# Kernel optimization log

Hardware: AMD Instinct MI355X
Metric: run time of the kernel (lower is better)

## Reference

```python
import jax, jax.numpy as jnp
import numpy as np

D_MODEL = 512
NHEAD = 8
HEAD_DIM = D_MODEL // NHEAD
D_FF = 2048
EPS = 1e-5


def _linear_params(key, d_in, d_out):
    kw, kb = jax.random.split(key)
    bound = 1.0 / np.sqrt(d_in)
    W = jax.random.uniform(kw, (d_out, d_in), jnp.float32, -bound, bound)
    b = jax.random.uniform(kb, (d_out,), jnp.float32, -bound, bound)
    return W, b


def setup_inputs() -> dict:
    key = jax.random.key(0)
    ks = jax.random.split(key, 8)
    src = jax.random.normal(ks[0], (4, 2048, D_MODEL), jnp.float32)
    Wq, bq = _linear_params(ks[1], D_MODEL, D_MODEL)
    Wk, bk = _linear_params(ks[2], D_MODEL, D_MODEL)
    Wv, bv = _linear_params(ks[3], D_MODEL, D_MODEL)
    Wo, bo = _linear_params(ks[4], D_MODEL, D_MODEL)
    W1, b1 = _linear_params(ks[5], D_MODEL, D_FF)
    W2, b2 = _linear_params(ks[6], D_FF, D_MODEL)
    g1 = jnp.ones((D_MODEL,), jnp.float32)
    be1 = jnp.zeros((D_MODEL,), jnp.float32)
    g2 = jnp.ones((D_MODEL,), jnp.float32)
    be2 = jnp.zeros((D_MODEL,), jnp.float32)
    return dict(src=src, Wq=Wq, bq=bq, Wk=Wk, bk=bk, Wv=Wv, bv=bv,
                Wo=Wo, bo=bo, W1=W1, b1=b1, W2=W2, b2=b2,
                g1=g1, be1=be1, g2=g2, be2=be2)


def _layer_norm(x, g, b):
    mu = jnp.mean(x, axis=-1, keepdims=True)
    var = jnp.mean(jnp.square(x - mu), axis=-1, keepdims=True)
    return (x - mu) / jnp.sqrt(var + EPS) * g + b


def reference(src, Wq, bq, Wk, bk, Wv, bv, Wo, bo, W1, b1, W2, b2, g1, be1, g2, be2):
    B, T, D = src.shape
    scale = np.sqrt(HEAD_DIM).astype(np.float32)
    # Projections (torch Linear: x @ W.T + b)
    Q = (src @ Wq.T + bq).reshape(B, T, NHEAD, HEAD_DIM).transpose(0, 2, 1, 3)
    K = (src @ Wk.T + bk).reshape(B, T, NHEAD, HEAD_DIM).transpose(0, 2, 1, 3)
    V = (src @ Wv.T + bv).reshape(B, T, NHEAD, HEAD_DIM).transpose(0, 2, 1, 3)
    # Explicit QK^T -> softmax -> V (no mask, dropout=0)
    scores = jnp.einsum('bhqd,bhkd->bhqk', Q, K) / scale  # (B,H,T,T)
    attn = jax.nn.softmax(scores, axis=-1)
    ctx = jnp.einsum('bhqk,bhkd->bhqd', attn, V)
    ctx = ctx.transpose(0, 2, 1, 3).reshape(B, T, D)
    attn_out = ctx @ Wo.T + bo
    # Add & Norm 1
    x = _layer_norm(src + attn_out, g1, be1)
    # FFN: Linear -> GELU -> Linear
    h = jax.nn.gelu(x @ W1.T + b1, approximate=False)
    ffn_out = h @ W2.T + b2
    # Add & Norm 2
    return _layer_norm(x + ffn_out, g2, be2)
```

## Files before the change

kernel.cpp:

```cpp
#include <hip/hip_runtime.h>
#include <hip/hip_bf16.h>
#include <hip/hip_fp16.h>
#include <math.h>

typedef __bf16 bf16_t;
typedef __bf16 bf16x8 __attribute__((ext_vector_type(8)));
typedef __bf16 bf16x2 __attribute__((ext_vector_type(2)));
typedef float  f32x4  __attribute__((ext_vector_type(4)));

#define D_MODEL 512
#define NHEAD   8
#define HD      64
#define D_FF    2048
#define TOKENS  8192
#define SEQ     2048
#define BATCH   4

__device__ __forceinline__ void gload16(const bf16_t* g, bf16_t* l)
{
    __builtin_amdgcn_global_load_lds(
        (const __attribute__((address_space(1))) void*)g,
        (__attribute__((address_space(3))) void*)l,
        16, 0, 0);
}

__device__ __forceinline__ void cvt4(const float* s, bf16_t* d)
{
    float4 v = *(const float4*)s;
    alignas(8) bf16_t t[4] = {(bf16_t)v.x, (bf16_t)v.y, (bf16_t)v.z, (bf16_t)v.w};
    *(uint2*)d = *(const uint2*)t;
}

__device__ __forceinline__ void barrier_raw() { asm volatile("s_barrier" ::: "memory"); }

__global__ void cvt_weights(const float* __restrict__ src,
                            const float* __restrict__ Wq, const float* __restrict__ Wk,
                            const float* __restrict__ Wv, const float* __restrict__ Wo,
                            const float* __restrict__ W1, const float* __restrict__ W2,
                            const float* __restrict__ bq, const float* __restrict__ bk,
                            const float* __restrict__ bv,
                            bf16_t* __restrict__ Xb,
                            bf16_t* __restrict__ Wqkvb, bf16_t* __restrict__ Wob,
                            bf16_t* __restrict__ W1b, bf16_t* __restrict__ W2b,
                            float* __restrict__ bqkv, float* __restrict__ zbias)
{
    int i = blockIdx.x * 256 + threadIdx.x;
    if (i < 1048576) { cvt4(src + (size_t)i * 4, Xb + (size_t)i * 4); return; }
    i -= 1048576;
    if (i < 65536)        cvt4(Wq + (size_t)i * 4,            Wqkvb + (size_t)i * 4);
    else if (i < 131072)  cvt4(Wk + (size_t)(i - 65536) * 4,  Wqkvb + (size_t)i * 4);
    else if (i < 196608)  cvt4(Wv + (size_t)(i - 131072) * 4, Wqkvb + (size_t)i * 4);
    else if (i < 262144)  cvt4(Wo + (size_t)(i - 196608) * 4, Wob + (size_t)(i - 196608) * 4);
    else if (i < 524288)  cvt4(W1 + (size_t)(i - 262144) * 4, W1b + (size_t)(i - 262144) * 4);
    else if (i < 786432)  cvt4(W2 + (size_t)(i - 524288) * 4, W2b + (size_t)(i - 524288) * 4);
    else if (i < 786816) {
        int j = i - 786432;
        const float* s = (j < 128) ? bq + j * 4 : (j < 256) ? bk + (j - 128) * 4
                                                            : bv + (j - 256) * 4;
        *(float4*)(bqkv + (j & 127) * 4 + (j >> 7) * 512) = *(const float4*)s;
    } else if (i < 786944) {
        int j = i - 786816;
        *(float4*)(zbias + j * 4) = make_float4(0.f, 0.f, 0.f, 0.f);
    }
}

template <int EPI>
__global__ __launch_bounds__(512, 2)
void gemm256(const bf16_t* __restrict__ A, const bf16_t* __restrict__ B,
             const float* __restrict__ bias, bf16_t* __restrict__ C,
             int M, int N, int K)
{
    __shared__ bf16_t sA[2][256][64];
    __shared__ bf16_t sB[2][256][64];
    bf16_t* sAf = &sA[0][0][0];
    bf16_t* sBf = &sB[0][0][0];

    const int tid  = threadIdx.x;
    const int wave = tid >> 6;
    const int lane = tid & 63;
    const int g    = lane >> 4;
    const int c16  = lane & 15;
    const int wm   = (wave >> 2) * 128;
    const int wn   = (wave & 3) * 64;

    const int nwg  = gridDim.x * gridDim.y;
    const int flat = blockIdx.y * gridDim.x + blockIdx.x;
    const int swz  = (flat & 7) * (nwg >> 3) + (flat >> 3);
    const int m0   = (swz / gridDim.x) * 256;
    const int n0   = (swz % gridDim.x) * 256;

    const f32x4 fz = {0.f, 0.f, 0.f, 0.f};
    f32x4 acc[8][4];
#pragma unroll
    for (int i = 0; i < 8; i++)
#pragma unroll
        for (int j = 0; j < 4; j++) acc[i][j] = fz;

    const bf16_t* gA[4]; const bf16_t* gB[4]; int fa[4];
#pragma unroll
    for (int i = 0; i < 4; i++) {
        const int f = i * 512 + tid, row = f >> 3, l = (f & 7) ^ (row & 7);
        fa[i] = f;
        gA[i] = A + (size_t)(m0 + row) * K + l * 8;
        gB[i] = B + (size_t)(n0 + row) * K + l * 8;
    }

    auto stage = [&](int ko, int buf) {
        bf16_t* dA = sAf + buf * (256 * 64);
        bf16_t* dB = sBf + buf * (256 * 64);
#pragma unroll
        for (int i = 0; i < 4; i++) gload16(gA[i] + ko, dA + fa[i] * 8);
#pragma unroll
        for (int i = 0; i < 4; i++) gload16(gB[i] + ko, dB + fa[i] * 8);
    };

    stage(0, 0);
    stage(64, 1);

    const int NS = K >> 6;
    for (int s = 0; s < NS; ++s) {
        const int cur = s & 1;
        if (s + 1 < NS) asm volatile("s_waitcnt vmcnt(8)" ::: "memory");
        else            asm volatile("s_waitcnt vmcnt(0)" ::: "memory");
        barrier_raw();

#pragma unroll
        for (int ks = 0; ks < 2; ++ks) {
            const int ck = ((ks * 4 + g) ^ (c16 & 7)) * 8;
            bf16x8 af[8], bfr[4];
#pragma unroll
            for (int i = 0; i < 8; i++)
                af[i] = *(const bf16x8*)&sA[cur][wm + i * 16 + c16][ck];
#pragma unroll
            for (int j = 0; j < 4; j++)
                bfr[j] = *(const bf16x8*)&sB[cur][wn + j * 16 + c16][ck];
#pragma unroll
            for (int mi = 0; mi < 8; mi++)
#pragma unroll
                for (int ni = 0; ni < 4; ni++)
                    acc[mi][ni] = __builtin_amdgcn_mfma_f32_16x16x32_bf16(
                        af[mi], bfr[ni], acc[mi][ni], 0, 0, 0);
        }

        barrier_raw();
        if (s + 2 < NS) stage((s + 2) << 6, cur);
    }

    float bcol[4];
#pragma unroll
    for (int ni = 0; ni < 4; ni++) bcol[ni] = bias[n0 + wn + ni * 16 + c16];
#pragma unroll
    for (int mi = 0; mi < 8; mi++) {
#pragma unroll
        for (int ni = 0; ni < 4; ni++) {
            const int col = n0 + wn + ni * 16 + c16;
#pragma unroll
            for (int r = 0; r < 4; r++) {
                const int row = m0 + wm + mi * 16 + g * 4 + r;
                float v = acc[mi][ni][r] + bcol[ni];
                if (EPI == 1) v = 0.5f * v * (1.f + erff(v * 0.70710678118654752f));
                C[(size_t)row * N + col] = (bf16_t)v;
            }
        }
    }
}

template <int BM, int EPI, bool SPLIT2>
__global__ __launch_bounds__(256)
void gemm_bt(const bf16_t* __restrict__ A, const bf16_t* __restrict__ B,
             const float* __restrict__ bias, const float* __restrict__ biasz,
             void* __restrict__ Cout, int M, int N, int K)
{
    constexpr int MI = BM / 32;
    constexpr int NA = BM / 32;
    __shared__ bf16_t sA[2][BM][64];
    __shared__ bf16_t sB[2][128][64];
    bf16_t* sAf = &sA[0][0][0];
    bf16_t* sBf = &sB[0][0][0];

    const int tid  = threadIdx.x;
    const int wave = tid >> 6;
    const int lane = tid & 63;
    const int g    = lane >> 4;
    const int c16  = lane & 15;
    const int wm   = (wave >> 1) * (BM / 2);
    const int wn   = (wave & 1) * 64;
    const int m0   = blockIdx.y * BM;
    const int n0   = blockIdx.x * 128;

    const int zz    = SPLIT2 ? blockIdx.z : 0;
    const int Keff  = SPLIT2 ? (K >> 1) : K;
    const int kbase = zz * Keff;
    const float* bptr = (SPLIT2 && zz) ? biasz : bias;

    const f32x4 fz = {0.f, 0.f, 0.f, 0.f};
    f32x4 acc[MI][4];
#pragma unroll
    for (int i = 0; i < MI; i++)
#pragma unroll
        for (int j = 0; j < 4; j++) acc[i][j] = fz;

    const bf16_t* gA[NA]; int fa[NA];
#pragma unroll
    for (int i = 0; i < NA; i++) {
        const int f = i * 256 + tid, row = f >> 3, l = (f & 7) ^ (row & 7);
        fa[i] = f;
        gA[i] = A + (size_t)(m0 + row) * K + kbase + l * 8;
    }
    const bf16_t* gB[4]; int fb[4];
#pragma unroll
    for (int i = 0; i < 4; i++) {
        const int f = i * 256 + tid, row = f >> 3, l = (f & 7) ^ (row & 7);
        fb[i] = f;
        gB[i] = B + (size_t)(n0 + row) * K + kbase + l * 8;
    }

#pragma unroll
    for (int i = 0; i < NA; i++) gload16(gA[i], sAf + fa[i] * 8);
#pragma unroll
    for (int i = 0; i < 4; i++)  gload16(gB[i], sBf + fb[i] * 8);

    const int NS = Keff >> 6;
    for (int s = 0; s < NS; ++s) {
        const int cur = s & 1;
        __syncthreads();
        if (s + 1 < NS) {
            const int ko = (s + 1) * 64;
            bf16_t* dA = sAf + (cur ^ 1) * (BM * 64);
            bf16_t* dB = sBf + (cur ^ 1) * 8192;
#pragma unroll
            for (int i = 0; i < NA; i++) gload16(gA[i] + ko, dA + fa[i] * 8);
#pragma unroll
            for (int i = 0; i < 4; i++)  gload16(gB[i] + ko, dB + fb[i] * 8);
        }

#pragma unroll
        for (int sub = 0; sub < 2; ++sub) {
            const int ck = (((sub * 4 + g) ^ (c16 & 7))) * 8;
            bf16x8 af[MI], bfr[4];
#pragma unroll
            for (int i = 0; i < MI; i++)
                af[i] = *(const bf16x8*)&sA[cur][wm + i * 16 + c16][ck];
#pragma unroll
            for (int j = 0; j < 4; j++)
                bfr[j] = *(const bf16x8*)&sB[cur][wn + j * 16 + c16][ck];
#pragma unroll
            for (int mi = 0; mi < MI; mi++)
#pragma unroll
                for (int ni = 0; ni < 4; ni++)
                    acc[mi][ni] = __builtin_amdgcn_mfma_f32_16x16x32_bf16(
                        af[mi], bfr[ni], acc[mi][ni], 0, 0, 0);
        }
    }

    __half* outh = (__half*)Cout + (size_t)zz * M * N;
#pragma unroll
    for (int mi = 0; mi < MI; mi++) {
#pragma unroll
        for (int ni = 0; ni < 4; ni++) {
            const int col = n0 + wn + ni * 16 + c16;
            const float bv = bptr[col];
#pragma unroll
            for (int r = 0; r < 4; r++) {
                const int row = m0 + wm + mi * 16 + g * 4 + r;
                float v = acc[mi][ni][r] + bv;
                if (EPI == 1) v = 0.5f * v * (1.f + erff(v * 0.70710678118654752f));
                if (EPI == 2)
                    outh[(size_t)row * N + col] = (__half)v;
                else
                    ((bf16_t*)Cout)[(size_t)row * N + col] = (bf16_t)v;
            }
        }
    }
}

__global__ __launch_bounds__(256)
void transpose_v(const bf16_t* __restrict__ qkv, bf16_t* __restrict__ vt)
{
    __shared__ bf16_t st[64][72];
    const int t0 = blockIdx.x * 64;
    const int bh = blockIdx.y;
    const int b = bh >> 3, h = bh & 7;
    const int tid = threadIdx.x;

    for (int c = tid; c < 512; c += 256) {
        int r = c >> 3, cj = (c & 7) * 8;
        const bf16_t* src = qkv + ((size_t)(b * SEQ + t0 + r)) * 1536 + 1024 + h * 64 + cj;
        *(int4*)&st[r][cj] = *(const int4*)src;
    }
    __syncthreads();
    for (int c = tid; c < 512; c += 256) {
        int d = c >> 3, pj = (c & 7) * 8;
        alignas(16) bf16_t tmp[8];
#pragma unroll
        for (int j = 0; j < 8; j++) {
            int p = pj + j;
            int t = ((p >> 5) << 5) + (((p >> 2) & 1) << 4) + (((p >> 3) & 3) << 2) + (p & 3);
            tmp[j] = st[t][d];
        }
        *(int4*)(vt + ((size_t)(bh * 64 + d)) * SEQ + t0 + pj) = *(const int4*)tmp;
    }
}

__global__ __launch_bounds__(256)
__attribute__((amdgpu_waves_per_eu(2, 2)))
void flash_attn(const bf16_t* __restrict__ qkv, const bf16_t* __restrict__ vt,
                bf16_t* __restrict__ ctx)
{
    __shared__ bf16_t sK[2][64][64];
    __shared__ bf16_t sVt[2][64][64];

    const int bh = blockIdx.y;
    const int b = bh >> 3, h = bh & 7;
    const int q0 = blockIdx.x * 128;
    const int tid = threadIdx.x;
    const int wave = tid >> 6, lane = tid & 63;
    const int g = lane >> 4, c16 = lane & 15;

    const float qscale = 0.125f * 1.4426950408889634f;
    bf16x8 aq[2][2];
#pragma unroll
    for (int qt = 0; qt < 2; qt++)
#pragma unroll
        for (int ks = 0; ks < 2; ks++) {
            bf16x8 v = *(const bf16x8*)(qkv +
                ((size_t)(b * SEQ + q0 + wave * 32 + qt * 16 + c16)) * 1536 +
                h * 64 + ks * 32 + g * 8);
#pragma unroll
            for (int j = 0; j < 8; j++) v[j] = (bf16_t)((float)v[j] * qscale);
            aq[qt][ks] = v;
        }

    const f32x4 fz = {0.f, 0.f, 0.f, 0.f};
    f32x4 acc_oT[4][2];
#pragma unroll
    for (int dt = 0; dt < 4; dt++)
#pragma unroll
        for (int qt = 0; qt < 2; qt++) acc_oT[dt][qt] = fz;
    float l_acc[2] = {0.f, 0.f};

    const int f0 = tid,        r0 = f0 >> 3, l0 = (f0 & 7) ^ (r0 & 7);
    const int f1 = tid + 256,  r1 = f1 >> 3, l1 = (f1 & 7) ^ (r1 & 7);
    const bf16_t* gK0 = qkv + ((size_t)(b * SEQ + r0)) * 1536 + 512 + h * 64 + l0 * 8;
    const bf16_t* gK1 = qkv + ((size_t)(b * SEQ + r1)) * 1536 + 512 + h * 64 + l1 * 8;
    const bf16_t* gV0 = vt + ((size_t)(bh * 64 + r0)) * SEQ + l0 * 8;
    const bf16_t* gV1 = vt + ((size_t)(bh * 64 + r1)) * SEQ + l1 * 8;
    bf16_t* lK = &sK[0][0][0];
    bf16_t* lV = &sVt[0][0][0];

    gload16(gK0, lK + f0 * 8);
    gload16(gK1, lK + f1 * 8);
    gload16(gV0, lV + f0 * 8);
    gload16(gV1, lV + f1 * 8);

    for (int it = 0; it < 32; ++it) {
        const int cur = it & 1;
        __syncthreads();
        if (it < 31) {
            const size_t kv = (size_t)(it + 1) * 64;
            const int bo = (cur ^ 1) * 4096;
            gload16(gK0 + kv * 1536, lK + bo + f0 * 8);
            gload16(gK1 + kv * 1536, lK + bo + f1 * 8);
            gload16(gV0 + kv,        lV + bo + f0 * 8);
            gload16(gV1 + kv,        lV + bo + f1 * 8);
        }

        f32x4 accs[4][2];
#pragma unroll
        for (int tt = 0; tt < 4; tt++)
#pragma unroll
            for (int qt = 0; qt < 2; qt++) accs[tt][qt] = fz;
#pragma unroll
        for (int ks = 0; ks < 2; ks++) {
            const int pc = ((ks * 4 + g) ^ (c16 & 7)) * 8;
#pragma unroll
            for (int tt = 0; tt < 4; tt++) {
                bf16x8 ak = *(const bf16x8*)&sK[cur][tt * 16 + c16][pc];
                accs[tt][0] = __builtin_amdgcn_mfma_f32_16x16x32_bf16(ak, aq[0][ks], accs[tt][0], 0, 0, 0);
                accs[tt][1] = __builtin_amdgcn_mfma_f32_16x16x32_bf16(ak, aq[1][ks], accs[tt][1], 0, 0, 0);
            }
        }

#pragma unroll
        for (int tt = 0; tt < 4; tt++)
#pragma unroll
            for (int qt = 0; qt < 2; qt++) {
                float s = 0.f;
#pragma unroll
                for (int r = 0; r < 4; r++) {
                    float p = __builtin_amdgcn_exp2f(accs[tt][qt][r]);
                    accs[tt][qt][r] = p;
                    s += p;
                }
                l_acc[qt] += s;
            }
        bf16x8 pb[2][2];
#pragma unroll
        for (int qt = 0; qt < 2; qt++)
#pragma unroll
            for (int kv = 0; kv < 2; kv++)
#pragma unroll
                for (int j = 0; j < 8; j++)
                    pb[qt][kv][j] = (bf16_t)accs[kv * 2 + (j >> 2)][qt][j & 3];

#pragma unroll
        for (int kv = 0; kv < 2; kv++) {
            const int pc = ((kv * 4 + g) ^ (c16 & 7)) * 8;
#pragma unroll
            for (int dt = 0; dt < 4; dt++) {
                bf16x8 av = *(const bf16x8*)&sVt[cur][dt * 16 + c16][pc];
                acc_oT[dt][0] = __builtin_amdgcn_mfma_f32_16x16x32_bf16(av, pb[0][kv], acc_oT[dt][0], 0, 0, 0);
                acc_oT[dt][1] = __builtin_amdgcn_mfma_f32_16x16x32_bf16(av, pb[1][kv], acc_oT[dt][1], 0, 0, 0);
            }
        }
    }

#pragma unroll
    for (int qt = 0; qt < 2; qt++) {
        float l = l_acc[qt];
        l += __shfl_xor(l, 16);
        l += __shfl_xor(l, 32);
        const float inv = 1.0f / l;
        const int token = q0 + wave * 32 + qt * 16 + c16;
        bf16_t* dst = ctx + ((size_t)(b * SEQ + token)) * 512 + h * 64 + g * 4;
#pragma unroll
        for (int dt = 0; dt < 4; dt++) {
            alignas(8) bf16_t o4[4];
#pragma unroll
            for (int r = 0; r < 4; r++) o4[r] = (bf16_t)(acc_oT[dt][qt][r] * inv);
            *(uint2*)(dst + dt * 16) = *(const uint2*)o4;
        }
    }
}

__global__ __launch_bounds__(256)
void add_ln3(const float* __restrict__ a, const __half* __restrict__ b,
             const __half* __restrict__ c,
             const float* __restrict__ gamma, const float* __restrict__ beta,
             float* __restrict__ outf, bf16_t* __restrict__ outb)
{
    const int row  = blockIdx.x * 4 + (threadIdx.x >> 6);
    const int lane = threadIdx.x & 63;
    const size_t base = (size_t)row * 512 + lane * 8;

    int4 braw = *(const int4*)(b + base);
    int4 craw = *(const int4*)(c + base);
    const __half* bh = (const __half*)&braw;
    const __half* ch = (const __half*)&craw;

    float v[8];
#pragma unroll
    for (int hh = 0; hh < 2; hh++) {
        float4 av = *(const float4*)(a + base + hh * 4);
        v[hh * 4 + 0] = av.x + (float)bh[hh * 4 + 0] + (float)ch[hh * 4 + 0];
        v[hh * 4 + 1] = av.y + (float)bh[hh * 4 + 1] + (float)ch[hh * 4 + 1];
        v[hh * 4 + 2] = av.z + (float)bh[hh * 4 + 2] + (float)ch[hh * 4 + 2];
        v[hh * 4 + 3] = av.w + (float)bh[hh * 4 + 3] + (float)ch[hh * 4 + 3];
    }

    float s = 0.f;
#pragma unroll
    for (int i = 0; i < 8; i++) s += v[i];
#pragma unroll
    for (int off = 32; off > 0; off >>= 1) s += __shfl_xor(s, off);
    const float mu = s * (1.f / 512.f);

    float q = 0.f;
#pragma unroll
    for (int i = 0; i < 8; i++) { float d = v[i] - mu; q += d * d; }
#pragma unroll
    for (int off = 32; off > 0; off >>= 1) q += __shfl_xor(q, off);
    const float rstd = rsqrtf(q * (1.f / 512.f) + 1e-5f);

    float4 g0 = *(const float4*)(gamma + lane * 8);
    float4 g1 = *(const float4*)(gamma + lane * 8 + 4);
    float4 e0 = *(const float4*)(beta + lane * 8);
    float4 e1 = *(const float4*)(beta + lane * 8 + 4);
    const float gg[8] = {g0.x, g0.y, g0.z, g0.w, g1.x, g1.y, g1.z, g1.w};
    const float ee[8] = {e0.x, e0.y, e0.z, e0.w, e1.x, e1.y, e1.z, e1.w};

    float o[8];
#pragma unroll
    for (int i = 0; i < 8; i++) o[i] = (v[i] - mu) * rstd * gg[i] + ee[i];

    *(float4*)(outf + base)     = make_float4(o[0], o[1], o[2], o[3]);
    *(float4*)(outf + base + 4) = make_float4(o[4], o[5], o[6], o[7]);
    if (outb) {
        alignas(16) bf16_t ob[8];
#pragma unroll
        for (int i = 0; i < 8; i++) ob[i] = (bf16_t)o[i];
        *(int4*)(outb + base) = *(const int4*)ob;
    }
}

extern "C" void kernel_launch(void* const* d_in, const int* in_sizes, int n_in,
                              void* d_out, int out_size, void* d_ws, size_t ws_size,
                              hipStream_t stream)
{
    const float* src = (const float*)d_in[0];
    const float* Wq  = (const float*)d_in[1];  const float* bq  = (const float*)d_in[2];
    const float* Wk  = (const float*)d_in[3];  const float* bk  = (const float*)d_in[4];
    const float* Wv  = (const float*)d_in[5];  const float* bv  = (const float*)d_in[6];
    const float* Wo  = (const float*)d_in[7];  const float* bo  = (const float*)d_in[8];
    const float* W1  = (const float*)d_in[9];  const float* b1  = (const float*)d_in[10];
    const float* W2  = (const float*)d_in[11]; const float* b2  = (const float*)d_in[12];
    const float* g1  = (const float*)d_in[13]; const float* be1 = (const float*)d_in[14];
    const float* g2  = (const float*)d_in[15]; const float* be2 = (const float*)d_in[16];
    float* out = (float*)d_out;

    char* ws = (char*)d_ws;
    size_t off = 0;
    auto alloc = [&](size_t bytes) -> void* {
        void* p = ws + off;
        off = (off + bytes + 255) & ~(size_t)255;
        return p;
    };

    bf16_t* Xb    = (bf16_t*)alloc((size_t)TOKENS * 512 * 2);
    bf16_t* Wqkvb = (bf16_t*)alloc((size_t)1536 * 512 * 2);
    bf16_t* Wob   = (bf16_t*)alloc((size_t)512 * 512 * 2);
    bf16_t* W1b   = (bf16_t*)alloc((size_t)2048 * 512 * 2);
    bf16_t* W2b   = (bf16_t*)alloc((size_t)512 * 2048 * 2);
    float*  bqkv  = (float*)alloc(1536 * 4);
    float*  zbias = (float*)alloc(512 * 4);
    bf16_t* QKV   = (bf16_t*)alloc((size_t)TOKENS * 1536 * 2);
    bf16_t* Vt    = (bf16_t*)alloc((size_t)32 * 64 * SEQ * 2);
    bf16_t* CTX   = (bf16_t*)alloc((size_t)TOKENS * 512 * 2);
    __half* ATTa  = (__half*)alloc((size_t)TOKENS * 512 * 2);
    __half* ATTb  = (__half*)alloc((size_t)TOKENS * 512 * 2);
    float*  X1    = (float*)alloc((size_t)TOKENS * 512 * 4);
    bf16_t* X1b   = (bf16_t*)alloc((size_t)TOKENS * 512 * 2);

    bf16_t* H    = QKV;
    __half* FFNa = ATTa;
    __half* FFNb = ATTb;

    cvt_weights<<<7170, 256, 0, stream>>>(src, Wq, Wk, Wv, Wo, W1, W2, bq, bk, bv,
                                          Xb, Wqkvb, Wob, W1b, W2b, bqkv, zbias);

    gemm256<0><<<dim3(6, 32), 512, 0, stream>>>(
        Xb, Wqkvb, bqkv, QKV, TOKENS, 1536, 512);

    transpose_v<<<dim3(32, 32), 256, 0, stream>>>(QKV, Vt);
    flash_attn<<<dim3(16, 32), 256, 0, stream>>>(QKV, Vt, CTX);

    gemm_bt<64, 2, true><<<dim3(4, 128, 2), 256, 0, stream>>>(
        CTX, Wob, bo, zbias, ATTa, TOKENS, 512, 512);

    add_ln3<<<2048, 256, 0, stream>>>(src, ATTa, ATTb, g1, be1, X1, X1b);

    gemm256<1><<<dim3(8, 32), 512, 0, stream>>>(
        X1b, W1b, b1, H, TOKENS, 2048, 512);

    gemm_bt<64, 2, true><<<dim3(4, 128, 2), 256, 0, stream>>>(
        H, W2b, b2, zbias, FFNa, TOKENS, 512, 2048);

    add_ln3<<<2048, 256, 0, stream>>>(X1, FFNa, FFNb, g2, be2, out, nullptr);
}
```

Measured before the change: 279.8 us.

## Deepen async global-to-LDS prefetch with explicit vmcnt waits and raw barriers

The GEMM kernel now issues two stages of global_load_lds up front and, each iteration, waits with a partial vmcnt and a raw barrier instead of __syncthreads. It issues the next-next stage after compute, behind a second barrier, so loads stay in flight across compute. Flash attention moves to a three-buffer K/V ring with a prefetch distance of two tiles and adds s_setprio around the MFMA blocks. The cost targeted is load latency exposed by the full vmcnt drain implied by __syncthreads. In exchange it uses more LDS, adds an extra barrier per GEMM iteration, and relies on hand-counted vmcnt values that must match the number of loads issued per stage.

```diff
diff --git a/kernel.cpp b/kernel.cpp
--- a/kernel.cpp
+++ b/kernel.cpp
@@ -215,24 +215,28 @@
         gB[i] = B + (size_t)(n0 + row) * K + kbase + l * 8;
     }
 
-#pragma unroll
-    for (int i = 0; i < NA; i++) gload16(gA[i], sAf + fa[i] * 8);
-#pragma unroll
-    for (int i = 0; i < 4; i++)  gload16(gB[i], sBf + fb[i] * 8);
+    auto stage = [&](int ko, int buf) {
+        bf16_t* dA = sAf + buf * (BM * 64);
+        bf16_t* dB = sBf + buf * 8192;
+#pragma unroll
+        for (int i = 0; i < NA; i++) gload16(gA[i] + ko, dA + fa[i] * 8);
+#pragma unroll
+        for (int i = 0; i < 4; i++)  gload16(gB[i] + ko, dB + fb[i] * 8);
+    };
+
+    stage(0, 0);
+    stage(64, 1);
 
     const int NS = Keff >> 6;
     for (int s = 0; s < NS; ++s) {
         const int cur = s & 1;
-        __syncthreads();
         if (s + 1 < NS) {
-            const int ko = (s + 1) * 64;
-            bf16_t* dA = sAf + (cur ^ 1) * (BM * 64);
-            bf16_t* dB = sBf + (cur ^ 1) * 8192;
-#pragma unroll
-            for (int i = 0; i < NA; i++) gload16(gA[i] + ko, dA + fa[i] * 8);
-#pragma unroll
-            for (int i = 0; i < 4; i++)  gload16(gB[i] + ko, dB + fb[i] * 8);
-        }
+            if constexpr (NA == 2) asm volatile("s_waitcnt vmcnt(6)" ::: "memory");
+            else                   asm volatile("s_waitcnt vmcnt(8)" ::: "memory");
+        } else {
+            asm volatile("s_waitcnt vmcnt(0)" ::: "memory");
+        }
+        barrier_raw();
 
 #pragma unroll
         for (int sub = 0; sub < 2; ++sub) {
@@ -251,6 +255,9 @@
                     acc[mi][ni] = __builtin_amdgcn_mfma_f32_16x16x32_bf16(
                         af[mi], bfr[ni], acc[mi][ni], 0, 0, 0);
         }
+
+        barrier_raw();
+        if (s + 2 < NS) stage((s + 2) << 6, cur);
     }
 
     __half* outh = (__half*)Cout + (size_t)zz * M * N;
@@ -307,8 +314,8 @@
 void flash_attn(const bf16_t* __restrict__ qkv, const bf16_t* __restrict__ vt,
                 bf16_t* __restrict__ ctx)
 {
-    __shared__ bf16_t sK[2][64][64];
-    __shared__ bf16_t sVt[2][64][64];
+    __shared__ bf16_t sK[3][64][64];
+    __shared__ bf16_t sVt[3][64][64];
 
     const int bh = blockIdx.y;
     const int b = bh >> 3, h = bh & 7;
@@ -348,28 +355,30 @@
     bf16_t* lK = &sK[0][0][0];
     bf16_t* lV = &sVt[0][0][0];
 
-    gload16(gK0, lK + f0 * 8);
-    gload16(gK1, lK + f1 * 8);
-    gload16(gV0, lV + f0 * 8);
-    gload16(gV1, lV + f1 * 8);
+    auto stageKV = [&](int t) {
+        const int bo = (t % 3) * 4096;
+        const size_t kv = (size_t)t * 64;
+        gload16(gK0 + kv * 1536, lK + bo + f0 * 8);
+        gload16(gK1 + kv * 1536, lK + bo + f1 * 8);
+        gload16(gV0 + kv,        lV + bo + f0 * 8);
+        gload16(gV1 + kv,        lV + bo + f1 * 8);
+    };
+
+    stageKV(0);
+    stageKV(1);
 
     for (int it = 0; it < 32; ++it) {
-        const int cur = it & 1;
-        __syncthreads();
-        if (it < 31) {
-            const size_t kv = (size_t)(it + 1) * 64;
-            const int bo = (cur ^ 1) * 4096;
-            gload16(gK0 + kv * 1536, lK + bo + f0 * 8);
-            gload16(gK1 + kv * 1536, lK + bo + f1 * 8);
-            gload16(gV0 + kv,        lV + bo + f0 * 8);
-            gload16(gV1 + kv,        lV + bo + f1 * 8);
-        }
+        const int cur = it % 3;
+        if (it < 31) asm volatile("s_waitcnt vmcnt(4)" ::: "memory");
+        else         asm volatile("s_waitcnt vmcnt(0)" ::: "memory");
+        barrier_raw();
 
         f32x4 accs[4][2];
 #pragma unroll
         for (int tt = 0; tt < 4; tt++)
 #pragma unroll
             for (int qt = 0; qt < 2; qt++) accs[tt][qt] = fz;
+        __builtin_amdgcn_s_setprio(1);
 #pragma unroll
         for (int ks = 0; ks < 2; ks++) {
             const int pc = ((ks * 4 + g) ^ (c16 & 7)) * 8;
@@ -380,6 +389,7 @@
                 accs[tt][1] = __builtin_amdgcn_mfma_f32_16x16x32_bf16(ak, aq[1][ks], accs[tt][1], 0, 0, 0);
             }
         }
+        __builtin_amdgcn_s_setprio(0);
 
 #pragma unroll
         for (int tt = 0; tt < 4; tt++)
@@ -403,6 +413,7 @@
                 for (int j = 0; j < 8; j++)
                     pb[qt][kv][j] = (bf16_t)accs[kv * 2 + (j >> 2)][qt][j & 3];
 
+        __builtin_amdgcn_s_setprio(1);
 #pragma unroll
         for (int kv = 0; kv < 2; kv++) {
             const int pc = ((kv * 4 + g) ^ (c16 & 7)) * 8;
@@ -413,6 +424,9 @@
                 acc_oT[dt][1] = __builtin_amdgcn_mfma_f32_16x16x32_bf16(av, pb[1][kv], acc_oT[dt][1], 0, 0, 0);
             }
         }
+        __builtin_amdgcn_s_setprio(0);
+
+        if (it + 2 < 32) stageKV(it + 2);
     }
 
 #pragma unroll
```

New measurement: 273.6 us. 1.02x faster.
